# Performance work log

Measured on AMD Instinct MI355X. Metric: run time of the kernel, lower is better.

Reference implementation:

```python
import jax, jax.numpy as jnp
import numpy as np

VOCAB, E, H = 53, 16, 32
B, S = 4096, 512


def setup_inputs() -> dict:
    key = jax.random.key(0)
    k = jax.random.split(key, 8)
    x = jax.random.randint(k[0], (B, S), 0, VOCAB)
    emb = jax.random.normal(k[1], (VOCAB, E), jnp.float32) * 0.1
    emb = emb.at[0].set(0.0)  # padding_idx=0 row is zero
    s = 1.0 / np.sqrt(H).astype(np.float32)
    W_ih = jax.random.uniform(k[2], (4 * H, E), jnp.float32, -s, s)
    W_hh = jax.random.uniform(k[3], (4 * H, H), jnp.float32, -s, s)
    b_ih = jax.random.uniform(k[4], (4 * H,), jnp.float32, -s, s)
    b_hh = jax.random.uniform(k[5], (4 * H,), jnp.float32, -s, s)
    sf = 1.0 / np.sqrt(H).astype(np.float32)
    W_fc = jax.random.uniform(k[6], (1, H), jnp.float32, -sf, sf)
    b_fc = jax.random.uniform(k[7], (1,), jnp.float32, -sf, sf)
    return {"x": x, "emb": emb, "W_ih": W_ih, "W_hh": W_hh,
            "b_ih": b_ih, "b_hh": b_hh, "W_fc": W_fc, "b_fc": b_fc}


def _lstm_last_hidden(ex, W_ih, W_hh, b_ih, b_hh):
    # ex: [B,S,E]. Precompute input contribution to all 4 gates: [B,S,4H]
    xg = jnp.einsum('bse,ge->bsg', ex, W_ih) + (b_ih + b_hh)
    b = ex.shape[0]
    h0 = jnp.zeros((b, H), ex.dtype)
    c0 = jnp.zeros((b, H), ex.dtype)

    def step(carry, xt):
        h, c = carry
        g = xt + h @ W_hh.T  # [B,4H]; torch gate order i,f,g,o
        i, f, gg, o = jnp.split(g, 4, axis=-1)
        c = jax.nn.sigmoid(f) * c + jax.nn.sigmoid(i) * jnp.tanh(gg)
        h = jax.nn.sigmoid(o) * jnp.tanh(c)
        return (h, c), None

    (hT, _), _ = jax.lax.scan(step, (h0, c0), jnp.swapaxes(xg, 0, 1))
    return hT  # [B,H]


def reference(x, emb, W_ih, W_hh, b_ih, b_hh, W_fc, b_fc):
    ex = emb[x]  # [B,S,E] embedding lookup
    hT = _lstm_last_hidden(ex, W_ih, W_hh, b_ih, b_hh)
    out = hT @ W_fc.T + b_fc  # [B,1]
    return jax.nn.sigmoid(out).squeeze()  # [B]
```

## Files before the change

kernel.cpp:

```cpp
#include <hip/hip_runtime.h>

#define VOCAB 53
#define EDIM  16
#define H     32
#define SEQ   512
#define BATCH 4096
#define LOG2E 1.4426950408889634f
#define XRS   132
#define HS    72
#define RSC   2048.0f
#define RSCI  (1.0f/2048.0f)

typedef _Float16 f16x8 __attribute__((ext_vector_type(8)));
typedef float f32x4 __attribute__((ext_vector_type(4)));

__device__ __forceinline__ float exp2_hw(float x) {
    float r; asm("v_exp_f32 %0, %1" : "=v"(r) : "v"(x)); return r;
}
__device__ __forceinline__ float sig_exp2(float xs) {
    return __builtin_amdgcn_rcpf(1.0f + exp2_hw(xs));
}

__device__ __forceinline__ void decode_row(int rp, int& orig, float& scale) {
    int m = rp >> 4, rem = rp & 15, s = rem >> 2, g = rem & 3;
    orig = g * 32 + 4 * m + s;
    scale = (g == 2) ? (-2.0f * LOG2E) : (-LOG2E);
}

__device__ __forceinline__ int pi_slot_unit(int s) {
    return 8 * (s >> 3) + 4 * (s & 1) + ((s >> 1) & 3);
}

__global__ __launch_bounds__(512, 1)
void lstm_seq_classifier(const int* __restrict__ x,
                         const float* __restrict__ emb,
                         const float* __restrict__ W_ih,
                         const float* __restrict__ W_hh,
                         const float* __restrict__ b_ih,
                         const float* __restrict__ b_hh,
                         const float* __restrict__ W_fc,
                         const float* __restrict__ b_fc,
                         float* __restrict__ out) {
    __shared__ float xg_perm[VOCAB * XRS];
    __shared__ _Float16 whi[128 * 32];
    __shared__ _Float16 wlo[128 * 32];
    __shared__ __align__(16) _Float16 hhi_buf[2][16][HS];
    __shared__ __align__(16) _Float16 hlo_buf[2][16][HS];
    __shared__ float red[16 * 33];

    const int tid  = threadIdx.x;
    const int lane = tid & 63;
    const int w    = tid >> 6;
    const int col  = lane & 15;
    const int q    = lane >> 4;

    for (int idx = tid; idx < VOCAB * 128; idx += 512) {
        int v = idx >> 7, rp = idx & 127;
        int orig; float scale; decode_row(rp, orig, scale);
        float acc = b_ih[orig] + b_hh[orig];
        const float* ev = emb + v * EDIM;
        const float* wr = W_ih + orig * EDIM;
#pragma unroll
        for (int e = 0; e < EDIM; ++e) acc += ev[e] * wr[e];
        xg_perm[v * XRS + rp] = scale * acc;
    }
    for (int idx = tid; idx < 128 * 32; idx += 512) {
        int rp = idx >> 5, k = idx & 31;
        int orig; float scale; decode_row(rp, orig, scale);
        int ku = pi_slot_unit(k);
        float wv = scale * W_hh[orig * H + ku];
        _Float16 hi = (_Float16)wv;
        whi[idx] = hi;
        wlo[idx] = (_Float16)((wv - (float)hi) * RSC);
    }
    for (int idx = tid; idx < 2 * 16 * HS; idx += 512) {
        (&hhi_buf[0][0][0])[idx] = (_Float16)0.f;
        (&hlo_buf[0][0][0])[idx] = (_Float16)0.f;
    }
    __syncthreads();

    const f16x8 Ahi = *reinterpret_cast<const f16x8*>(&whi[(16 * w + col) * 32 + 8 * q]);
    const f16x8 Alo = *reinterpret_cast<const f16x8*>(&wlo[(16 * w + col) * 32 + 8 * q]);

    const long xb = (long)(blockIdx.x * 16 + col) * SEQ;
    const int xoff = 16 * w + 4 * q;
    const int wslot = 2 * q + (w & 1) + 8 * (w >> 1);
    int vc = x[xb + 1];
    f32x4 xg_cur = *reinterpret_cast<const f32x4*>(&xg_perm[x[xb] * XRS + xoff]);

    float ccs = 0.0f, h = 0.0f;
    const f32x4 zeroC = {0.f, 0.f, 0.f, 0.f};

    for (int s = 0; s < SEQ; ++s) {
        const int rb = s & 1, nb = rb ^ 1;
        f16x8 Bhi = *reinterpret_cast<const f16x8*>(&hhi_buf[rb][col][8 * q]);
        f16x8 Blo = *reinterpret_cast<const f16x8*>(&hlo_buf[rb][col][8 * q]);

        f32x4 D   = __builtin_amdgcn_mfma_f32_16x16x32_f16(Ahi, Bhi, xg_cur, 0, 0, 0);
        f32x4 Dra = __builtin_amdgcn_mfma_f32_16x16x32_f16(Alo, Bhi, zeroC, 0, 0, 0);
        f32x4 Drb = __builtin_amdgcn_mfma_f32_16x16x32_f16(Ahi, Blo, zeroC, 0, 0, 0);

        __builtin_amdgcn_sched_barrier(0);
        f32x4 xg_nxt = *reinterpret_cast<const f32x4*>(&xg_perm[vc * XRS + xoff]);
        int vn = x[xb + ((s + 2) & (SEQ - 1))];

        float zi = __builtin_fmaf(RSCI, Dra[0] + Drb[0], D[0]);
        float zf = __builtin_fmaf(RSCI, Dra[1] + Drb[1], D[1]);
        float zg = __builtin_fmaf(RSCI, Dra[2] + Drb[2], D[2]);
        float zo = __builtin_fmaf(RSCI, Dra[3] + Drb[3], D[3]);

        float si = sig_exp2(zi);
        float sf = sig_exp2(zf);
        float ug = sig_exp2(zg);
        float so = sig_exp2(zo);
        float t1 = __builtin_fmaf(-4.0f * LOG2E, ug, 2.0f * LOG2E);
        ccs = __builtin_fmaf(sf, ccs, si * t1);
        float tc = __builtin_fmaf(2.0f, sig_exp2(ccs), -1.0f);
        h = so * tc;

        _Float16 hf = (_Float16)h;
        hhi_buf[nb][col][wslot] = hf;
        hlo_buf[nb][col][wslot] = (_Float16)((h - (float)hf) * RSC);

        asm volatile("s_waitcnt lgkmcnt(0)" ::: "memory");
        __builtin_amdgcn_s_barrier();

        xg_cur = xg_nxt;
        vc = vn;
    }

    red[col * 33 + 4 * w + q] = h * W_fc[4 * w + q];
    __syncthreads();
    if (w == 0) {
        const float* rr = &red[col * 33];
        float p = 0.f;
#pragma unroll
        for (int u = 0; u < 8; ++u) p += rr[8 * q + u];
        p += __shfl_xor(p, 16);
        p += __shfl_xor(p, 32);
        if (lane < 16) {
            out[blockIdx.x * 16 + col] = sig_exp2(-LOG2E * (p + b_fc[0]));
        }
    }
}

extern "C" void kernel_launch(void* const* d_in, const int* in_sizes, int n_in,
                              void* d_out, int out_size, void* d_ws, size_t ws_size,
                              hipStream_t stream) {
    const int*   x    = (const int*)d_in[0];
    const float* emb  = (const float*)d_in[1];
    const float* W_ih = (const float*)d_in[2];
    const float* W_hh = (const float*)d_in[3];
    const float* b_ih = (const float*)d_in[4];
    const float* b_hh = (const float*)d_in[5];
    const float* W_fc = (const float*)d_in[6];
    const float* b_fc = (const float*)d_in[7];
    float* out = (float*)d_out;

    dim3 grid(BATCH / 16);
    dim3 block(512);
    lstm_seq_classifier<<<grid, block, 0, stream>>>(x, emb, W_ih, W_hh,
                                                    b_ih, b_hh, W_fc, b_fc, out);
}
```

Baseline: 163.5 us.

## Drop low-part split of hidden state and simplify h exchange layout

Keeps only the fp16 high part of the hidden state. This removes the hlo buffer, its LDS store and load, and the third MFMA (Ahi×Blo) on each timestep's serial chain. It also drops the permuted W_hh column mapping and the custom write slot, so h is stored at unit index 4w+q. The next-token and xg prefetch loads move to the top of the loop, and the explicit waitcnt plus s_barrier becomes __syncthreads. The trade-off is that h is now rounded to fp16 at every step, which can let error build up over the 512-step recurrence.

```diff
diff --git a/kernel.cpp b/kernel.cpp
--- a/kernel.cpp
+++ b/kernel.cpp
@@ -27,10 +27,6 @@
     scale = (g == 2) ? (-2.0f * LOG2E) : (-LOG2E);
 }
 
-__device__ __forceinline__ int pi_slot_unit(int s) {
-    return 8 * (s >> 3) + 4 * (s & 1) + ((s >> 1) & 3);
-}
-
 __global__ __launch_bounds__(512, 1)
 void lstm_seq_classifier(const int* __restrict__ x,
                          const float* __restrict__ emb,
@@ -45,7 +41,6 @@
     __shared__ _Float16 whi[128 * 32];
     __shared__ _Float16 wlo[128 * 32];
     __shared__ __align__(16) _Float16 hhi_buf[2][16][HS];
-    __shared__ __align__(16) _Float16 hlo_buf[2][16][HS];
     __shared__ float red[16 * 33];
 
     const int tid  = threadIdx.x;
@@ -67,16 +62,13 @@
     for (int idx = tid; idx < 128 * 32; idx += 512) {
         int rp = idx >> 5, k = idx & 31;
         int orig; float scale; decode_row(rp, orig, scale);
-        int ku = pi_slot_unit(k);
-        float wv = scale * W_hh[orig * H + ku];
+        float wv = scale * W_hh[orig * H + k];
         _Float16 hi = (_Float16)wv;
         whi[idx] = hi;
         wlo[idx] = (_Float16)((wv - (float)hi) * RSC);
     }
-    for (int idx = tid; idx < 2 * 16 * HS; idx += 512) {
+    for (int idx = tid; idx < 2 * 16 * HS; idx += 512)
         (&hhi_buf[0][0][0])[idx] = (_Float16)0.f;
-        (&hlo_buf[0][0][0])[idx] = (_Float16)0.f;
-    }
     __syncthreads();
 
     const f16x8 Ahi = *reinterpret_cast<const f16x8*>(&whi[(16 * w + col) * 32 + 8 * q]);
@@ -84,7 +76,6 @@
 
     const long xb = (long)(blockIdx.x * 16 + col) * SEQ;
     const int xoff = 16 * w + 4 * q;
-    const int wslot = 2 * q + (w & 1) + 8 * (w >> 1);
     int vc = x[xb + 1];
     f32x4 xg_cur = *reinterpret_cast<const f32x4*>(&xg_perm[x[xb] * XRS + xoff]);
 
@@ -92,22 +83,19 @@
     const f32x4 zeroC = {0.f, 0.f, 0.f, 0.f};
 
     for (int s = 0; s < SEQ; ++s) {
+        int vn = x[xb + ((s + 2) & (SEQ - 1))];
+        f32x4 xg_nxt = *reinterpret_cast<const f32x4*>(
+            &xg_perm[vc * XRS + xoff]);
         const int rb = s & 1, nb = rb ^ 1;
         f16x8 Bhi = *reinterpret_cast<const f16x8*>(&hhi_buf[rb][col][8 * q]);
-        f16x8 Blo = *reinterpret_cast<const f16x8*>(&hlo_buf[rb][col][8 * q]);
 
         f32x4 D   = __builtin_amdgcn_mfma_f32_16x16x32_f16(Ahi, Bhi, xg_cur, 0, 0, 0);
         f32x4 Dra = __builtin_amdgcn_mfma_f32_16x16x32_f16(Alo, Bhi, zeroC, 0, 0, 0);
-        f32x4 Drb = __builtin_amdgcn_mfma_f32_16x16x32_f16(Ahi, Blo, zeroC, 0, 0, 0);
 
-        __builtin_amdgcn_sched_barrier(0);
-        f32x4 xg_nxt = *reinterpret_cast<const f32x4*>(&xg_perm[vc * XRS + xoff]);
-        int vn = x[xb + ((s + 2) & (SEQ - 1))];
-
-        float zi = __builtin_fmaf(RSCI, Dra[0] + Drb[0], D[0]);
-        float zf = __builtin_fmaf(RSCI, Dra[1] + Drb[1], D[1]);
-        float zg = __builtin_fmaf(RSCI, Dra[2] + Drb[2], D[2]);
-        float zo = __builtin_fmaf(RSCI, Dra[3] + Drb[3], D[3]);
+        float zi = __builtin_fmaf(RSCI, Dra[0], D[0]);
+        float zf = __builtin_fmaf(RSCI, Dra[1], D[1]);
+        float zg = __builtin_fmaf(RSCI, Dra[2], D[2]);
+        float zo = __builtin_fmaf(RSCI, Dra[3], D[3]);
 
         float si = sig_exp2(zi);
         float sf = sig_exp2(zf);
@@ -118,13 +106,8 @@
         float tc = __builtin_fmaf(2.0f, sig_exp2(ccs), -1.0f);
         h = so * tc;
 
-        _Float16 hf = (_Float16)h;
-        hhi_buf[nb][col][wslot] = hf;
-        hlo_buf[nb][col][wslot] = (_Float16)((h - (float)hf) * RSC);
-
-        asm volatile("s_waitcnt lgkmcnt(0)" ::: "memory");
-        __builtin_amdgcn_s_barrier();
-
+        hhi_buf[nb][col][4 * w + q] = (_Float16)h;
+        __syncthreads();
         xg_cur = xg_nxt;
         vc = vn;
     }
```

Measured after the change: 147.0 us, median of 2. -10.1%, faster.
